# Kernel optimization log

Measured on AMD Instinct MI355X. Metric: run time of the kernel, lower is better.

## Reference

```python
import jax, jax.numpy as jnp
import numpy as np

N_NODES = 100000
N_EDGES = 1600000
N_GRAPHS = 64
VOCAB = 50000
D = 128
EPS = 1e-5


def setup_inputs() -> dict:
    key = jax.random.key(0)
    ks = jax.random.split(key, 24)
    tokens = jax.random.randint(ks[0], (N_NODES,), 0, VOCAB)
    src = jax.random.randint(ks[1], (N_EDGES,), 0, N_NODES)
    dst = jax.random.randint(ks[2], (N_EDGES,), 0, N_NODES)
    graph_ids = jnp.sort(jax.random.randint(ks[3], (N_NODES,), 0, N_GRAPHS))
    s = 1.0 / np.sqrt(D)
    inp = {
        'tokens': tokens, 'src': src, 'dst': dst, 'graph_ids': graph_ids,
        'embed': jax.random.normal(ks[4], (VOCAB, D), jnp.float32),
        'W1': jax.random.normal(ks[5], (D, D), jnp.float32) * s,
        'b1': jnp.zeros((D,), jnp.float32),
        'g1': jnp.ones((D,), jnp.float32), 'be1': jnp.zeros((D,), jnp.float32),
        'W2': jax.random.normal(ks[6], (D, D), jnp.float32) * s,
        'b2': jnp.zeros((D,), jnp.float32),
        'g2': jnp.ones((D,), jnp.float32), 'be2': jnp.zeros((D,), jnp.float32),
        'W3': jax.random.normal(ks[7], (D, D), jnp.float32) * s,
        'b3': jnp.zeros((D,), jnp.float32),
        'g3': jnp.ones((D,), jnp.float32), 'be3': jnp.zeros((D,), jnp.float32),
        'fcW1': jax.random.normal(ks[8], (D, D // 2), jnp.float32) * s,
        'fcb1': jnp.zeros((D // 2,), jnp.float32),
        'fcW2': jax.random.normal(ks[9], (D // 2, 2), jnp.float32) * (1.0 / np.sqrt(D // 2)),
        'fcb2': jnp.zeros((2,), jnp.float32),
    }
    return inp


def _graph_conv(h, src, dst, norm_src, norm_dst, W, b):
    # DGL GraphConv, norm='both': D_out^{-1/2} -> sum-aggregate -> D_in^{-1/2} -> linear
    msg = (h * norm_src[:, None])[src]                      # [E, D]
    agg = jax.ops.segment_sum(msg, dst, num_segments=N_NODES)
    return (agg * norm_dst[:, None]) @ W + b


def _bn_relu(h, gamma, beta):
    mu = jnp.mean(h, axis=0)
    var = jnp.mean((h - mu) ** 2, axis=0)                   # biased var (torch BN)
    return jax.nn.relu((h - mu) * jax.lax.rsqrt(var + EPS) * gamma + beta)


def reference(tokens, src, dst, graph_ids, embed,
              W1, b1, g1, be1, W2, b2, g2, be2, W3, b3, g3, be3,
              fcW1, fcb1, fcW2, fcb2):
    ones_e = jnp.ones((N_EDGES,), jnp.float32)
    deg_out = jnp.maximum(jax.ops.segment_sum(ones_e, src, num_segments=N_NODES), 1.0)
    deg_in = jnp.maximum(jax.ops.segment_sum(ones_e, dst, num_segments=N_NODES), 1.0)
    norm_src = jax.lax.rsqrt(deg_out)
    norm_dst = jax.lax.rsqrt(deg_in)

    h = embed[tokens]                                        # [N, D]
    h = _bn_relu(_graph_conv(h, src, dst, norm_src, norm_dst, W1, b1), g1, be1)
    h = _bn_relu(_graph_conv(h, src, dst, norm_src, norm_dst, W2, b2), g2, be2)
    h = _bn_relu(_graph_conv(h, src, dst, norm_src, norm_dst, W3, b3), g3, be3)

    # dgl.mean_nodes per graph
    sums = jax.ops.segment_sum(h, graph_ids, num_segments=N_GRAPHS)  # [G, D]
    cnts = jnp.maximum(jax.ops.segment_sum(jnp.ones((N_NODES,), jnp.float32), graph_ids, num_segments=N_GRAPHS), 1.0)
    hg = sums / cnts[:, None]

    hg = jax.nn.relu(hg @ fcW1 + fcb1)                       # dropout = identity (eval)
    return hg @ fcW2 + fcb2                                  # [G, 2]
```

## Files before the change

### kernel.cpp

```cpp
#include <hip/hip_runtime.h>

#define N_NODES 100000
#define N_EDGES 1600000
#define N_GRAPHS 64
#define DIM 128
#define BN_EPS 1e-5f
#define EPAD 2000000

#define NB_SENT 977
#define NB_WPREP 192
#define NB_HIST 391
#define NB_ZERO 40
#define NBUCK 782
#define NG (NBUCK * NB_HIST)
#define NB_SCANG2 2389
#define BUCK_RESERVE 388

#define AT_STRIDE 136

typedef unsigned short ushort_t;
typedef unsigned char uchar_t;
typedef unsigned int uint_t;
typedef __attribute__((ext_vector_type(8))) short bf16x8;
typedef __attribute__((ext_vector_type(4))) float f32x4;

__device__ __forceinline__ float bfl(uint_t u) {
    union { uint_t i; float f; } v; v.i = u << 16; return v.f;
}
__device__ __forceinline__ float bfh(uint_t u) {
    union { uint_t i; float f; } v; v.i = u & 0xffff0000u; return v.f;
}
__device__ __forceinline__ ushort_t f2bf(float f) {
    union { float f; uint_t i; } v; v.f = f;
    uint_t x = v.i;
    return (ushort_t)((x + 0x7fffu + ((x >> 16) & 1u)) >> 16);
}
__device__ __forceinline__ uint_t pack2(float lo, float hi) {
    return ((uint_t)f2bf(hi) << 16) | (uint_t)f2bf(lo);
}

__global__ void k_front(const int* __restrict__ src, const int* __restrict__ dst,
                        ushort_t* __restrict__ bufA, int* __restrict__ esrc,
                        const float* __restrict__ w1, const float* __restrict__ w2,
                        const float* __restrict__ w3, ushort_t* __restrict__ wbt,
                        int* __restrict__ GG, int* __restrict__ zp, int zwords) {
    __shared__ int hh[NBUCK];
    __shared__ int hh2[NBUCK];
    int b = blockIdx.x;
    int t = threadIdx.x;
    if (b < NB_SENT) {
        int i0 = (b * 256 + t) * 8;
        int4 sv = make_int4(N_NODES, N_NODES, N_NODES, N_NODES);
        if (i0 + 8 <= EPAD) {
            *(int4*)(esrc + i0) = sv;
            *(int4*)(esrc + i0 + 4) = sv;
        } else {
            for (int i = i0; i < EPAD; ++i) esrc[i] = N_NODES;
        }
        if (b == 0 && t < 64)
            ((uint_t*)(bufA + (size_t)N_NODES * DIM))[t] = 0u;
        return;
    }
    b -= NB_SENT;
    if (b < NB_WPREP) {
        int i = b * 256 + t;
        int l = i >> 14;
        int idx = i & (DIM * DIM - 1);
        int n = idx >> 7, k = idx & (DIM - 1);
        const float* wsrc = (l == 0) ? w1 : (l == 1) ? w2 : w3;
        wbt[i] = f2bf(wsrc[k * DIM + n]);
        return;
    }
    b -= NB_WPREP;
    if (b < NB_HIST) {
        for (int k = t; k < NBUCK; k += 256) { hh[k] = 0; hh2[k] = 0; }
        __syncthreads();
        int e0 = b * 4096;
        int e1 = min(e0 + 4096, N_EDGES);
        for (int i = e0 + t; i < e1; i += 256) {
            atomicAdd(&hh[dst[i] >> 7], 1);
            atomicAdd(&hh2[src[i] >> 7], 1);
        }
        __syncthreads();
        for (int k = t; k < NBUCK; k += 256) {
            GG[k * NB_HIST + b] = hh[k];
            GG[NG + k * NB_HIST + b] = hh2[k];
        }
        return;
    }
    b -= NB_HIST;
    {
        int i = b * 256 + t;
        if (i < zwords) zp[i] = 0;
    }
}

__global__ void k_scanA(const int* __restrict__ GG, int* __restrict__ Gs,
                        int* __restrict__ partials) {
    __shared__ int s[256];
    int t = threadIdx.x;
    int i = blockIdx.x * 256 + t;
    int v = (i < 2 * NG) ? GG[i] : 0;
    s[t] = v;
    __syncthreads();
    for (int off = 1; off < 256; off <<= 1) {
        int add = (t >= off) ? s[t - off] : 0;
        __syncthreads();
        s[t] += add;
        __syncthreads();
    }
    if (i < 2 * NG) Gs[i + 1] = s[t];
    if (t == 255) partials[blockIdx.x] = s[t];
}

__global__ void k_scanB(const int* __restrict__ partials, int* __restrict__ Gs) {
    __shared__ int s[256];
    int t = threadIdx.x;
    int p = 0;
    for (int j = t; j < (int)blockIdx.x; j += 256) p += partials[j];
    s[t] = p;
    __syncthreads();
    for (int off = 128; off > 0; off >>= 1) {
        if (t < off) s[t] += s[t + off];
        __syncthreads();
    }
    int prefix = s[0];
    int i = blockIdx.x * 256 + t;
    if (i < 2 * NG) Gs[i + 1] += prefix;
    if (blockIdx.x == 0 && t == 0) Gs[0] = 0;
}

__global__ void k_pass2(const int* __restrict__ src, const int* __restrict__ dst,
                        const int* __restrict__ Gs, uint_t* __restrict__ Cpk,
                        uchar_t* __restrict__ Cls) {
    __shared__ int cur[NBUCK];
    __shared__ int cur2[NBUCK];
    int b = blockIdx.x;
    int t = threadIdx.x;
    for (int k = t; k < NBUCK; k += 256) {
        cur[k] = Gs[k * NB_HIST + b];
        cur2[k] = Gs[NG + k * NB_HIST + b] - N_EDGES;
    }
    __syncthreads();
    int e0 = b * 4096;
    int e1 = min(e0 + 4096, N_EDGES);
    for (int i = e0 + t; i < e1; i += 256) {
        int d = dst[i];
        int s = src[i];
        int slot = atomicAdd(&cur[d >> 7], 1);
        Cpk[slot] = (uint_t)s | ((uint_t)(d & 127) << 17);
        int slot2 = atomicAdd(&cur2[s >> 7], 1);
        Cls[slot2] = (uchar_t)(s & 127);
    }
}

__global__ void k_fine(const uint_t* __restrict__ Cpk, const uchar_t* __restrict__ Cls,
                       const int* __restrict__ Gs,
                       const int* __restrict__ tokens, const float* __restrict__ embed,
                       int* __restrict__ esrc, int* __restrict__ rowptr,
                       int* __restrict__ pdeg, float* __restrict__ ns,
                       float* __restrict__ nd, ushort_t* __restrict__ bufA) {
    __shared__ int hcnt[128];
    __shared__ int hstart[128];
    __shared__ float lns[128];
    int b = blockIdx.x;
    int t = threadIdx.x;
    if (b < NBUCK) {
        int k = b;
        int node0 = k * 128;
        int nn = min(128, N_NODES - node0);
        int S = Gs[k * NB_HIST];
        int E = Gs[(k + 1) * NB_HIST];
        if (t < 128) hcnt[t] = 0;
        __syncthreads();
        for (int i = S + t; i < E; i += 256) atomicAdd(&hcnt[Cpk[i] >> 17], 1);
        __syncthreads();
        if (t == 0) {
            int acc = 0;
            for (int n = 0; n < nn; ++n) {
                hstart[n] = acc;
                acc += (hcnt[n] + 3) & ~3;
            }
        }
        __syncthreads();
        int base = (k * BUCK_RESERVE + S + 3) & ~3;
        if (t < nn) {
            int node = node0 + t;
            rowptr[node] = base + hstart[t];
            pdeg[node] = (hcnt[t] + 3) & ~3;
            nd[node] = rsqrtf(fmaxf((float)hcnt[t], 1.0f));
        }
        __syncthreads();
        for (int i = S + t; i < E; i += 256) {
            uint_t pk = Cpk[i];
            int slot = atomicAdd(&hstart[pk >> 17], 1);
            esrc[base + slot] = (int)(pk & 0x1FFFFu);
        }
    } else {
        int k = b - NBUCK;
        int node0 = k * 128;
        int nn = min(128, N_NODES - node0);
        int S = Gs[NG + k * NB_HIST] - N_EDGES;
        int E = Gs[NG + (k + 1) * NB_HIST] - N_EDGES;
        if (t < 128) hcnt[t] = 0;
        __syncthreads();
        for (int i = S + t; i < E; i += 256) atomicAdd(&hcnt[Cls[i]], 1);
        __syncthreads();
        if (t < nn) {
            float v = rsqrtf(fmaxf((float)hcnt[t], 1.0f));
            ns[node0 + t] = v;
            lns[t] = v;
        }
        if (k == 0 && t == 0) ns[N_NODES] = 0.f;
        __syncthreads();
        for (int slot = t; slot < nn * 16; slot += 256) {
            int nloc = slot >> 4, sub = slot & 15;
            int node = node0 + nloc;
            float s = lns[nloc];
            const float* ep = embed + (size_t)tokens[node] * DIM + sub * 8;
            float4 a = *(const float4*)ep;
            float4 c = *(const float4*)(ep + 4);
            uint4 o;
            o.x = pack2(a.x * s, a.y * s);
            o.y = pack2(a.z * s, a.w * s);
            o.z = pack2(c.x * s, c.y * s);
            o.w = pack2(c.z * s, c.w * s);
            *(uint4*)(bufA + (size_t)node * DIM + sub * 8) = o;
        }
    }
}

__global__ void k_prescale(const ushort_t* __restrict__ yin, const float* __restrict__ ns,
                           const float* __restrict__ bnsum, const float* __restrict__ bnsq,
                           const float* __restrict__ g, const float* __restrict__ be,
                           ushort_t* __restrict__ xout) {
    __shared__ float sa[DIM], sc[DIM];
    int t = threadIdx.x;
    if (t < DIM) {
        float mu = bnsum[t] * (1.0f / N_NODES);
        float var = bnsq[t] * (1.0f / N_NODES) - mu * mu;
        float rstd = rsqrtf(var + BN_EPS);
        float a = g[t] * rstd;
        sa[t] = a;
        sc[t] = be[t] - mu * a;
    }
    __syncthreads();
    int gid = blockIdx.x * 256 + t;
    int node = gid >> 4, sub = gid & 15;
    float s = ns[node];
    uint4 u = *(const uint4*)(yin + (size_t)node * DIM + sub * 8);
    float v[8] = {bfl(u.x), bfh(u.x), bfl(u.y), bfh(u.y),
                  bfl(u.z), bfh(u.z), bfl(u.w), bfh(u.w)};
    const float* a = sa + sub * 8;
    const float* c = sc + sub * 8;
#pragma unroll
    for (int i = 0; i < 8; ++i) v[i] = fmaxf(fmaf(v[i], a[i], c[i]), 0.f) * s;
    uint4 o;
    o.x = pack2(v[0], v[1]); o.y = pack2(v[2], v[3]);
    o.z = pack2(v[4], v[5]); o.w = pack2(v[6], v[7]);
    *(uint4*)(xout + (size_t)node * DIM + sub * 8) = o;
}

__global__ __launch_bounds__(256) void k_agggemm(const ushort_t* __restrict__ hs,
        const int* __restrict__ rowptr, const int* __restrict__ pdeg,
        const int* __restrict__ esrc, const float* __restrict__ nd,
        const ushort_t* __restrict__ wbt, const float* __restrict__ bias,
        ushort_t* __restrict__ y,
        float* __restrict__ bnsum, float* __restrict__ bnsq) {
    __shared__ ushort_t at[64 * AT_STRIDE];
    __shared__ float csum[DIM], csq[DIM];
    int tid = threadIdx.x;
    int wave = tid >> 6;
    int lane = tid & 63;
    if (tid < DIM) { csum[tid] = 0.f; csq[tid] = 0.f; }
    __syncthreads();

    int bnode = blockIdx.x * 64 + wave * 16;
    int off = lane * 2;

    int rpv = 0, pdv = 0;
    if (lane < 16) {
        int nnode = bnode + lane;
        if (nnode < N_NODES) { rpv = rowptr[nnode]; pdv = pdeg[nnode]; }
    }

#define LD2(s) (*(const uint_t*)(hs + (size_t)(s) * DIM + off))
#define ACC8(I0, I1, X0, Y0, X1, Y1)                                           \
    {                                                                          \
        uint_t u0 = LD2(I0.x), u1 = LD2(I0.y), u2 = LD2(I0.z), u3 = LD2(I0.w); \
        uint_t u4 = LD2(I1.x), u5 = LD2(I1.y), u6 = LD2(I1.z), u7 = LD2(I1.w); \
        X0 += bfl(u0); Y0 += bfh(u0); X1 += bfl(u1); Y1 += bfh(u1);            \
        X0 += bfl(u2); Y0 += bfh(u2); X1 += bfl(u3); Y1 += bfh(u3);            \
        X0 += bfl(u4); Y0 += bfh(u4); X1 += bfl(u5); Y1 += bfh(u5);            \
        X0 += bfl(u6); Y0 += bfh(u6); X1 += bfl(u7); Y1 += bfh(u7);            \
    }
#define ACC4(I0, X0, Y0, X1, Y1)                                               \
    {                                                                          \
        uint_t u0 = LD2(I0.x), u1 = LD2(I0.y), u2 = LD2(I0.z), u3 = LD2(I0.w); \
        X0 += bfl(u0); Y0 += bfh(u0); X1 += bfl(u1); Y1 += bfh(u1);            \
        X0 += bfl(u2); Y0 += bfh(u2); X1 += bfl(u3); Y1 += bfh(u3);            \
    }

    for (int i = 0; i < 16; i += 2) {
        int nodeA = bnode + i;
        int nodeB = bnode + i + 1;
        int eA = __shfl(rpv, i);
        int endA = eA + __shfl(pdv, i);
        int eB = __shfl(rpv, i + 1);
        int endB = eB + __shfl(pdv, i + 1);
        float xA0 = 0.f, yA0 = 0.f, xA1 = 0.f, yA1 = 0.f;
        float xB0 = 0.f, yB0 = 0.f, xB1 = 0.f, yB1 = 0.f;
        if (eA + 8 <= endA && eB + 8 <= endB) {
            int4 cA0 = *(const int4*)(esrc + eA);
            int4 cA1 = *(const int4*)(esrc + eA + 4);
            int4 cB0 = *(const int4*)(esrc + eB);
            int4 cB1 = *(const int4*)(esrc + eB + 4);
            while (true) {
                int4 nA0 = *(const int4*)(esrc + eA + 8);
                int4 nA1 = *(const int4*)(esrc + eA + 12);
                int4 nB0 = *(const int4*)(esrc + eB + 8);
                int4 nB1 = *(const int4*)(esrc + eB + 12);
                ACC8(cA0, cA1, xA0, yA0, xA1, yA1);
                ACC8(cB0, cB1, xB0, yB0, xB1, yB1);
                eA += 8; eB += 8;
                if (!(eA + 8 <= endA && eB + 8 <= endB)) break;
                cA0 = nA0; cA1 = nA1; cB0 = nB0; cB1 = nB1;
            }
        }
        for (; eA + 8 <= endA; eA += 8) {
            int4 i0 = *(const int4*)(esrc + eA);
            int4 i1 = *(const int4*)(esrc + eA + 4);
            ACC8(i0, i1, xA0, yA0, xA1, yA1);
        }
        if (eA < endA) {
            int4 i0 = *(const int4*)(esrc + eA);
            ACC4(i0, xA0, yA0, xA1, yA1);
        }
        for (; eB + 8 <= endB; eB += 8) {
            int4 i0 = *(const int4*)(esrc + eB);
            int4 i1 = *(const int4*)(esrc + eB + 4);
            ACC8(i0, i1, xB0, yB0, xB1, yB1);
        }
        if (eB < endB) {
            int4 i0 = *(const int4*)(esrc + eB);
            ACC4(i0, xB0, yB0, xB1, yB1);
        }
        uint_t ovA = 0u, ovB = 0u;
        if (nodeA < N_NODES) {
            float n = nd[nodeA];
            ovA = pack2((xA0 + xA1) * n, (yA0 + yA1) * n);
        }
        if (nodeB < N_NODES) {
            float n = nd[nodeB];
            ovB = pack2((xB0 + xB1) * n, (yB0 + yB1) * n);
        }
        *(uint_t*)&at[(wave * 16 + i) * AT_STRIDE + off] = ovA;
        *(uint_t*)&at[(wave * 16 + i + 1) * AT_STRIDE + off] = ovB;
    }
#undef ACC8
#undef ACC4
#undef LD2

    int m16 = lane & 15;
    int quad = lane >> 4;
    f32x4 acc[8];
#pragma unroll
    for (int nb = 0; nb < 8; ++nb) acc[nb] = (f32x4)(0.f);

    const ushort_t* ap = &at[(wave * 16 + m16) * AT_STRIDE + quad * 8];
#pragma unroll
    for (int k0b = 0; k0b < 4; ++k0b) {
        bf16x8 af = *(const bf16x8*)(ap + k0b * 32);
#pragma unroll
        for (int nb = 0; nb < 8; ++nb) {
            int ncol = nb * 16 + m16;
            bf16x8 bfg = *(const bf16x8*)(wbt + (size_t)ncol * DIM + k0b * 32 + quad * 8);
            acc[nb] = __builtin_amdgcn_mfma_f32_16x16x32_bf16(af, bfg, acc[nb], 0, 0, 0);
        }
    }

#pragma unroll
    for (int nb = 0; nb < 8; ++nb) {
        int col = nb * 16 + m16;
        float bcol = bias[col];
        float ps = 0.f, pq = 0.f;
#pragma unroll
        for (int reg = 0; reg < 4; ++reg) {
            int r = bnode + quad * 4 + reg;
            if (r < N_NODES) {
                float v = acc[nb][reg] + bcol;
                ps += v; pq += v * v;
                y[(size_t)r * DIM + col] = f2bf(v);
            }
        }
        atomicAdd(&csum[col], ps);
        atomicAdd(&csq[col], pq);
    }
    __syncthreads();
    if (tid < DIM) {
        atomicAdd(&bnsum[tid], csum[tid]);
        atomicAdd(&bnsq[tid], csq[tid]);
    }
}

#define POOL_NODES 128
__global__ void k_pool(const ushort_t* __restrict__ yin, const int* __restrict__ gids,
                       const float* __restrict__ bnsum, const float* __restrict__ bnsq,
                       const float* __restrict__ g, const float* __restrict__ be,
                       float* __restrict__ pool, int* __restrict__ cnt) {
    __shared__ int h[N_GRAPHS];
    int col = threadIdx.x;
    float mu = bnsum[col] * (1.0f / N_NODES);
    float var = bnsq[col] * (1.0f / N_NODES) - mu * mu;
    float rstd = rsqrtf(var + BN_EPS);
    float a = g[col] * rstd;
    float c = be[col] - mu * a;
    if (col < N_GRAPHS) h[col] = 0;
    __syncthreads();
    int base = blockIdx.x * POOL_NODES;
    int end = min(base + POOL_NODES, N_NODES);
    for (int n = base + col; n < end; n += 128) atomicAdd(&h[gids[n]], 1);
    __syncthreads();
    if (col < N_GRAPHS && h[col]) atomicAdd(&cnt[col], h[col]);
    float acc = 0.f;
    int cur = gids[base];
    for (int n = base; n < end; ++n) {
        int gg = gids[n];
        if (gg != cur) {
            atomicAdd(&pool[(size_t)cur * DIM + col], acc);
            acc = 0.f;
            cur = gg;
        }
        uint_t u = *(const uint_t*)(yin + (size_t)n * DIM + (col & ~1));
        float v = (col & 1) ? bfh(u) : bfl(u);
        acc += fmaxf(fmaf(v, a, c), 0.f);
    }
    atomicAdd(&pool[(size_t)cur * DIM + col], acc);
}

__global__ void k_final(const float* __restrict__ pool, const int* __restrict__ cnt,
                        const float* __restrict__ fcW1, const float* __restrict__ fcb1,
                        const float* __restrict__ fcW2, const float* __restrict__ fcb2,
                        float* __restrict__ out) {
    __shared__ float hg[DIM];
    __shared__ float z[64];
    int g = blockIdx.x;
    int t = threadIdx.x;
    float cf = fmaxf((float)cnt[g], 1.0f);
    hg[t] = pool[(size_t)g * DIM + t] / cf;
    __syncthreads();
    if (t < 64) {
        float acc = fcb1[t];
        for (int k = 0; k < DIM; ++k)
            acc += hg[k] * fcW1[k * 64 + t];
        z[t] = fmaxf(acc, 0.f);
    }
    __syncthreads();
    if (t < 2) {
        float acc = fcb2[t];
        for (int k = 0; k < 64; ++k)
            acc += z[k] * fcW2[k * 2 + t];
        out[g * 2 + t] = acc;
    }
}

extern "C" void kernel_launch(void* const* d_in, const int* in_sizes, int n_in,
                              void* d_out, int out_size, void* d_ws, size_t ws_size,
                              hipStream_t stream) {
    const int* tokens = (const int*)d_in[0];
    const int* src = (const int*)d_in[1];
    const int* dst = (const int*)d_in[2];
    const int* gids = (const int*)d_in[3];
    const float* embed = (const float*)d_in[4];
    const float* W1 = (const float*)d_in[5];
    const float* b1 = (const float*)d_in[6];
    const float* g1 = (const float*)d_in[7];
    const float* be1 = (const float*)d_in[8];
    const float* W2 = (const float*)d_in[9];
    const float* b2 = (const float*)d_in[10];
    const float* g2 = (const float*)d_in[11];
    const float* be2 = (const float*)d_in[12];
    const float* W3 = (const float*)d_in[13];
    const float* b3 = (const float*)d_in[14];
    const float* g3 = (const float*)d_in[15];
    const float* be3 = (const float*)d_in[16];
    const float* fcW1 = (const float*)d_in[17];
    const float* fcb1 = (const float*)d_in[18];
    const float* fcW2 = (const float*)d_in[19];
    const float* fcb2 = (const float*)d_in[20];
    float* out = (float*)d_out;

    char* w = (char*)d_ws;
    auto alloc = [&](size_t bytes) {
        void* p = (void*)w;
        w += (bytes + 255) & ~(size_t)255;
        return p;
    };
    ushort_t* bufH = (ushort_t*)alloc((size_t)(N_NODES + 1) * DIM * 2);
    ushort_t* bufA = (ushort_t*)alloc((size_t)(N_NODES + 1) * DIM * 2);
    ushort_t* bufY = (ushort_t*)alloc((size_t)(N_NODES + 1) * DIM * 2);
    int* esrc = (int*)alloc((size_t)EPAD * 4);
    int* rowptr = (int*)alloc((size_t)N_NODES * 4);
    int* pdeg = (int*)alloc((size_t)N_NODES * 4);
    float* ns = (float*)alloc((size_t)(N_NODES + 1) * 4);
    float* nd = (float*)alloc((size_t)N_NODES * 4);
    ushort_t* wbt = (ushort_t*)alloc(3 * DIM * DIM * 2);
    int* GG = (int*)alloc((size_t)(2 * NG) * 4);
    int* Gs = (int*)alloc((size_t)(2 * NG + 1) * 4);
    int* partials = (int*)alloc(4096 * 4);
    uint_t* Cpk = (uint_t*)alloc((size_t)N_EDGES * 4);
    uchar_t* Cls = (uchar_t*)alloc((size_t)N_EDGES);
    char* zstart = w;
    float* bnsum = (float*)alloc(3 * DIM * 4);
    float* bnsq = (float*)alloc(3 * DIM * 4);
    float* pool = (float*)alloc((size_t)N_GRAPHS * DIM * 4);
    int* cnt = (int*)alloc((size_t)N_GRAPHS * 4);
    int zwords = (int)((size_t)(w - zstart) / 4);

    k_front<<<NB_SENT + NB_WPREP + NB_HIST + NB_ZERO, 256, 0, stream>>>(
        src, dst, bufA, esrc, W1, W2, W3, wbt, GG, (int*)zstart, zwords);
    k_scanA<<<NB_SCANG2, 256, 0, stream>>>(GG, Gs, partials);
    k_scanB<<<NB_SCANG2, 256, 0, stream>>>(partials, Gs);
    k_pass2<<<NB_HIST, 256, 0, stream>>>(src, dst, Gs, Cpk, Cls);
    k_fine<<<2 * NBUCK, 256, 0, stream>>>(Cpk, Cls, Gs, tokens, embed,
                                          esrc, rowptr, pdeg, ns, nd, bufA);

    int nb_fused = (N_NODES + 63) / 64;
    int nb_ps = 6250;

    k_agggemm<<<nb_fused, 256, 0, stream>>>(bufA, rowptr, pdeg, esrc, nd,
                                            wbt, b1, bufY, bnsum, bnsq);
    k_prescale<<<nb_ps, 256, 0, stream>>>(bufY, ns, bnsum, bnsq, g1, be1, bufA);
    k_agggemm<<<nb_fused, 256, 0, stream>>>(bufA, rowptr, pdeg, esrc, nd,
                                            wbt + (size_t)DIM * DIM, b2, bufH,
                                            bnsum + DIM, bnsq + DIM);
    k_prescale<<<nb_ps, 256, 0, stream>>>(bufH, ns, bnsum + DIM, bnsq + DIM, g2, be2, bufA);
    k_agggemm<<<nb_fused, 256, 0, stream>>>(bufA, rowptr, pdeg, esrc, nd,
                                            wbt + (size_t)2 * DIM * DIM, b3, bufY,
                                            bnsum + 2 * DIM, bnsq + 2 * DIM);

    k_pool<<<(N_NODES + POOL_NODES - 1) / POOL_NODES, DIM, 0, stream>>>(
        bufY, gids, bnsum + 2 * DIM, bnsq + 2 * DIM, g3, be3, pool, cnt);
    k_final<<<N_GRAPHS, DIM, 0, stream>>>(pool, cnt, fcW1, fcb1, fcW2, fcb2, out);
}
```

Baseline: 630.0 us.

## Split gather across lane quads with 16-byte feature loads and cross-quad reduction

```diff
diff --git a/kernel.cpp b/kernel.cpp
--- a/kernel.cpp
+++ b/kernel.cpp
@@ -261,7 +261,7 @@
     *(uint4*)(xout + (size_t)node * DIM + sub * 8) = o;
 }
 
-__global__ __launch_bounds__(256) void k_agggemm(const ushort_t* __restrict__ hs,
+__global__ __launch_bounds__(256, 5) void k_agggemm(const ushort_t* __restrict__ hs,
         const int* __restrict__ rowptr, const int* __restrict__ pdeg,
         const int* __restrict__ esrc, const float* __restrict__ nd,
         const ushort_t* __restrict__ wbt, const float* __restrict__ bias,
@@ -276,7 +276,10 @@
     __syncthreads();
 
     int bnode = blockIdx.x * 64 + wave * 16;
-    int off = lane * 2;
+    int quad = lane >> 4;
+    int m16 = lane & 15;
+
+    const ushort_t* hrow = hs + (size_t)m16 * 8;
 
     int rpv = 0, pdv = 0;
     if (lane < 16) {
@@ -284,85 +287,91 @@
         if (nnode < N_NODES) { rpv = rowptr[nnode]; pdv = pdeg[nnode]; }
     }
 
-#define LD2(s) (*(const uint_t*)(hs + (size_t)(s) * DIM + off))
-#define ACC8(I0, I1, X0, Y0, X1, Y1)                                           \
-    {                                                                          \
-        uint_t u0 = LD2(I0.x), u1 = LD2(I0.y), u2 = LD2(I0.z), u3 = LD2(I0.w); \
-        uint_t u4 = LD2(I1.x), u5 = LD2(I1.y), u6 = LD2(I1.z), u7 = LD2(I1.w); \
-        X0 += bfl(u0); Y0 += bfh(u0); X1 += bfl(u1); Y1 += bfh(u1);            \
-        X0 += bfl(u2); Y0 += bfh(u2); X1 += bfl(u3); Y1 += bfh(u3);            \
-        X0 += bfl(u4); Y0 += bfh(u4); X1 += bfl(u5); Y1 += bfh(u5);            \
-        X0 += bfl(u6); Y0 += bfh(u6); X1 += bfl(u7); Y1 += bfh(u7);            \
-    }
-#define ACC4(I0, X0, Y0, X1, Y1)                                               \
-    {                                                                          \
-        uint_t u0 = LD2(I0.x), u1 = LD2(I0.y), u2 = LD2(I0.z), u3 = LD2(I0.w); \
-        X0 += bfl(u0); Y0 += bfh(u0); X1 += bfl(u1); Y1 += bfh(u1);            \
-        X0 += bfl(u2); Y0 += bfh(u2); X1 += bfl(u3); Y1 += bfh(u3);            \
+#define FEATLD(ix) (*(const uint4*)(hrow + (size_t)(ix) * DIM))
+#define ACCU(F, A)                                                  \
+    {                                                               \
+        A[0] += bfl((F).x); A[1] += bfh((F).x);                     \
+        A[2] += bfl((F).y); A[3] += bfh((F).y);                     \
+        A[4] += bfl((F).z); A[5] += bfh((F).z);                     \
+        A[6] += bfl((F).w); A[7] += bfh((F).w);                     \
+    }
+#define DRAIN(E, T, A)                                              \
+    {                                                               \
+        if ((T) >= 2) {                                             \
+            int i0_ = esrc[E], i1_ = esrc[(E) + 4];                 \
+            (E) += 8; (T) -= 2;                                     \
+            uint4 f0_ = FEATLD(i0_), f1_ = FEATLD(i1_);             \
+            while ((T) >= 2) {                                      \
+                int j0_ = esrc[E], j1_ = esrc[(E) + 4];             \
+                (E) += 8; (T) -= 2;                                 \
+                ACCU(f0_, A); ACCU(f1_, A);                         \
+                f0_ = FEATLD(j0_); f1_ = FEATLD(j1_);               \
+            }                                                       \
+            ACCU(f0_, A); ACCU(f1_, A);                             \
+        }                                                           \
+        if (T) {                                                    \
+            int i0_ = esrc[E];                                      \
+            uint4 f0_ = FEATLD(i0_);                                \
+            ACCU(f0_, A);                                           \
+        }                                                           \
     }
 
     for (int i = 0; i < 16; i += 2) {
         int nodeA = bnode + i;
         int nodeB = bnode + i + 1;
-        int eA = __shfl(rpv, i);
-        int endA = eA + __shfl(pdv, i);
-        int eB = __shfl(rpv, i + 1);
-        int endB = eB + __shfl(pdv, i + 1);
-        float xA0 = 0.f, yA0 = 0.f, xA1 = 0.f, yA1 = 0.f;
-        float xB0 = 0.f, yB0 = 0.f, xB1 = 0.f, yB1 = 0.f;
-        if (eA + 8 <= endA && eB + 8 <= endB) {
-            int4 cA0 = *(const int4*)(esrc + eA);
-            int4 cA1 = *(const int4*)(esrc + eA + 4);
-            int4 cB0 = *(const int4*)(esrc + eB);
-            int4 cB1 = *(const int4*)(esrc + eB + 4);
-            while (true) {
-                int4 nA0 = *(const int4*)(esrc + eA + 8);
-                int4 nA1 = *(const int4*)(esrc + eA + 12);
-                int4 nB0 = *(const int4*)(esrc + eB + 8);
-                int4 nB1 = *(const int4*)(esrc + eB + 12);
-                ACC8(cA0, cA1, xA0, yA0, xA1, yA1);
-                ACC8(cB0, cB1, xB0, yB0, xB1, yB1);
-                eA += 8; eB += 8;
-                if (!(eA + 8 <= endA && eB + 8 <= endB)) break;
-                cA0 = nA0; cA1 = nA1; cB0 = nB0; cB1 = nB1;
+        int eA = __shfl(rpv, i) + quad;
+        int tA = __shfl(pdv, i) >> 2;
+        int eB = __shfl(rpv, i + 1) + quad;
+        int tB = __shfl(pdv, i + 1) >> 2;
+        float aA[8] = {0.f, 0.f, 0.f, 0.f, 0.f, 0.f, 0.f, 0.f};
+        float aB[8] = {0.f, 0.f, 0.f, 0.f, 0.f, 0.f, 0.f, 0.f};
+        if (tA >= 2 && tB >= 2) {
+            int iA0 = esrc[eA], iA1 = esrc[eA + 4];
+            int iB0 = esrc[eB], iB1 = esrc[eB + 4];
+            eA += 8; eB += 8; tA -= 2; tB -= 2;
+            uint4 fA0 = FEATLD(iA0), fA1 = FEATLD(iA1);
+            uint4 fB0 = FEATLD(iB0), fB1 = FEATLD(iB1);
+            while (tA >= 2 && tB >= 2) {
+                int jA0 = esrc[eA], jA1 = esrc[eA + 4];
+                int jB0 = esrc[eB], jB1 = esrc[eB + 4];
+                eA += 8; eB += 8; tA -= 2; tB -= 2;
+                ACCU(fA0, aA); ACCU(fA1, aA);
+                ACCU(fB0, aB); ACCU(fB1, aB);
+                fA0 = FEATLD(jA0); fA1 = FEATLD(jA1);
+                fB0 = FEATLD(jB0); fB1 = FEATLD(jB1);
             }
-        }
-        for (; eA + 8 <= endA; eA += 8) {
-            int4 i0 = *(const int4*)(esrc + eA);
-            int4 i1 = *(const int4*)(esrc + eA + 4);
-            ACC8(i0, i1, xA0, yA0, xA1, yA1);
-        }
-        if (eA < endA) {
-            int4 i0 = *(const int4*)(esrc + eA);
-            ACC4(i0, xA0, yA0, xA1, yA1);
-        }
-        for (; eB + 8 <= endB; eB += 8) {
-            int4 i0 = *(const int4*)(esrc + eB);
-            int4 i1 = *(const int4*)(esrc + eB + 4);
-            ACC8(i0, i1, xB0, yB0, xB1, yB1);
-        }
-        if (eB < endB) {
-            int4 i0 = *(const int4*)(esrc + eB);
-            ACC4(i0, xB0, yB0, xB1, yB1);
-        }
-        uint_t ovA = 0u, ovB = 0u;
-        if (nodeA < N_NODES) {
-            float n = nd[nodeA];
-            ovA = pack2((xA0 + xA1) * n, (yA0 + yA1) * n);
-        }
-        if (nodeB < N_NODES) {
-            float n = nd[nodeB];
-            ovB = pack2((xB0 + xB1) * n, (yB0 + yB1) * n);
-        }
-        *(uint_t*)&at[(wave * 16 + i) * AT_STRIDE + off] = ovA;
-        *(uint_t*)&at[(wave * 16 + i + 1) * AT_STRIDE + off] = ovB;
-    }
-#undef ACC8
-#undef ACC4
-#undef LD2
-
-    int m16 = lane & 15;
-    int quad = lane >> 4;
+            ACCU(fA0, aA); ACCU(fA1, aA);
+            ACCU(fB0, aB); ACCU(fB1, aB);
+        }
+        DRAIN(eA, tA, aA);
+        DRAIN(eB, tB, aB);
+#pragma unroll
+        for (int j = 0; j < 8; ++j) {
+            aA[j] += __shfl_xor(aA[j], 16);
+            aA[j] += __shfl_xor(aA[j], 32);
+            aB[j] += __shfl_xor(aB[j], 16);
+            aB[j] += __shfl_xor(aB[j], 32);
+        }
+        float nA = (nodeA < N_NODES) ? nd[nodeA] : 0.f;
+        float nB = (nodeB < N_NODES) ? nd[nodeB] : 0.f;
+        if (quad == 0) {
+            uint4 oA, oB;
+            oA.x = pack2(aA[0] * nA, aA[1] * nA);
+            oA.y = pack2(aA[2] * nA, aA[3] * nA);
+            oA.z = pack2(aA[4] * nA, aA[5] * nA);
+            oA.w = pack2(aA[6] * nA, aA[7] * nA);
+            oB.x = pack2(aB[0] * nB, aB[1] * nB);
+            oB.y = pack2(aB[2] * nB, aB[3] * nB);
+            oB.z = pack2(aB[4] * nB, aB[5] * nB);
+            oB.w = pack2(aB[6] * nB, aB[7] * nB);
+            *(uint4*)&at[(wave * 16 + i) * AT_STRIDE + m16 * 8] = oA;
+            *(uint4*)&at[(wave * 16 + i + 1) * AT_STRIDE + m16 * 8] = oB;
+        }
+    }
+#undef DRAIN
+#undef ACCU
+#undef FEATLD
+
     f32x4 acc[8];
 #pragma unroll
     for (int nb = 0; nb < 8; ++nb) acc[nb] = (f32x4)(0.f);
```

New measurement: 667.0 us. 1.06x slower.
